# Kernel tuning notes

Measured on AMD Instinct MI355X. Metric: run time of the kernel, lower is better.

The kernel has to match this reference:

```python
import jax, jax.numpy as jnp
import numpy as np

N = 50000          # nodes
E = 800000         # edges (avg degree 16)
D_IN, H1, H2, C = 512, 128, 64, 2
BN_EPS = 1e-5


def gcn_conv(x, w, b, src, dst, deg_inv_sqrt, n):
    """PyG GCNConv (eval): out = D^{-1/2}(A+I)D^{-1/2} (x @ w) + b.
    src/dst already include self-loops; deg_inv_sqrt precomputed on A+I."""
    h = x @ w                                        # [n, out_dim]
    norm = deg_inv_sqrt[src] * deg_inv_sqrt[dst]     # [E+n]
    msgs = h[src] * norm[:, None]                    # gather + scale
    out = jax.ops.segment_sum(msgs, dst, num_segments=n)  # scatter-add
    return out + b


def batch_norm(h, gamma, beta, mean, var):
    return (h - mean) * jax.lax.rsqrt(var + BN_EPS) * gamma + beta


def setup_inputs() -> dict:
    key = jax.random.key(0)
    ks = jax.random.split(key, 18)
    inp = {
        "x": jax.random.normal(ks[0], (N, D_IN), dtype=jnp.float32),
        "edge_index": jax.random.randint(ks[1], (2, E), 0, N, dtype=jnp.int64),
        # layer 1
        "w1": jax.random.normal(ks[2], (D_IN, H1), dtype=jnp.float32) / np.sqrt(D_IN),
        "b1": jnp.zeros((H1,), jnp.float32),
        "g1": jax.random.uniform(ks[3], (H1,), jnp.float32, 0.8, 1.2),
        "beta1": jax.random.normal(ks[4], (H1,), jnp.float32) * 0.1,
        "m1": jax.random.normal(ks[5], (H1,), jnp.float32) * 0.1,
        "v1": jax.random.uniform(ks[6], (H1,), jnp.float32, 0.5, 1.5),
        # layer 2
        "w2": jax.random.normal(ks[7], (H1, H2), dtype=jnp.float32) / np.sqrt(H1),
        "b2": jnp.zeros((H2,), jnp.float32),
        "g2": jax.random.uniform(ks[8], (H2,), jnp.float32, 0.8, 1.2),
        "beta2": jax.random.normal(ks[9], (H2,), jnp.float32) * 0.1,
        "m2": jax.random.normal(ks[10], (H2,), jnp.float32) * 0.1,
        "v2": jax.random.uniform(ks[11], (H2,), jnp.float32, 0.5, 1.5),
        # layer 3
        "w3": jax.random.normal(ks[12], (H2, C), dtype=jnp.float32) / np.sqrt(H2),
        "b3": jnp.zeros((C,), jnp.float32),
    }
    return inp


def reference(x, edge_index, w1, b1, g1, beta1, m1, v1,
              w2, b2, g2, beta2, m2, v2, w3, b3):
    n = x.shape[0]
    loops = jnp.arange(n, dtype=edge_index.dtype)
    src = jnp.concatenate([edge_index[0], loops])   # A + I
    dst = jnp.concatenate([edge_index[1], loops])
    deg = jax.ops.segment_sum(jnp.ones_like(dst, dtype=x.dtype), dst, num_segments=n)
    deg_inv_sqrt = jnp.where(deg > 0, jax.lax.rsqrt(deg), 0.0)

    h = gcn_conv(x, w1, b1, src, dst, deg_inv_sqrt, n)
    h = jax.nn.relu(batch_norm(h, g1, beta1, m1, v1))   # dropout is identity in eval
    h = gcn_conv(h, w2, b2, src, dst, deg_inv_sqrt, n)
    h = jax.nn.relu(batch_norm(h, g2, beta2, m2, v2))
    out = gcn_conv(h, w3, b3, src, dst, deg_inv_sqrt, n)
    return out
```

## Files before the change

### kernel.cpp

```cpp
#include <hip/hip_runtime.h>
#include <hip/hip_fp16.h>


constexpr int NN = 50000;
constexpr int NE = 800000;
constexpr float BN_EPS = 1e-5f;

using f16x8 = __attribute__((ext_vector_type(8))) _Float16;
using f32x4 = __attribute__((ext_vector_type(4))) float;

__global__ void k_prep(const float* __restrict__ w1,
                       const float* __restrict__ b1, const float* __restrict__ g1,
                       const float* __restrict__ beta1, const float* __restrict__ m1,
                       const float* __restrict__ v1,
                       const float* __restrict__ b2, const float* __restrict__ g2,
                       const float* __restrict__ beta2, const float* __restrict__ m2,
                       const float* __restrict__ v2,
                       __half* __restrict__ w1t,
                       float* __restrict__ bns1, float* __restrict__ bnb1,
                       float* __restrict__ bns2, float* __restrict__ bnb2) {
    int i = blockIdx.x * 256 + threadIdx.x;
    if (i < 512 * 128) {
        int k = i >> 7, n = i & 127;
        w1t[n * 512 + k] = __float2half(w1[i]);
    } else if (i < 512 * 128 + 128) {
        int f = i - 512 * 128;
        float s = g1[f] * rsqrtf(v1[f] + BN_EPS);
        bns1[f] = s;
        bnb1[f] = (b1[f] - m1[f]) * s + beta1[f];
    } else if (i < 512 * 128 + 128 + 64) {
        int f = i - (512 * 128 + 128);
        float s = g2[f] * rsqrtf(v2[f] + BN_EPS);
        bns2[f] = s;
        bnb2[f] = (b2[f] - m2[f]) * s + beta2[f];
    }
}


__global__ void k_count(const int* __restrict__ dst, int* __restrict__ cnt, int e) {
    int i = blockIdx.x * 256 + threadIdx.x;
    if (i < e) atomicAdd(&cnt[dst[i]], 1);
}

__global__ __launch_bounds__(1024) void k_scan(const int* __restrict__ cnt,
                                               int* __restrict__ row_start,
                                               float* __restrict__ dis, int n) {
    __shared__ int wsum[16];
    int tid = threadIdx.x;
    int lane = tid & 63, wv = tid >> 6;
    int running = 0;
    if (tid == 0) row_start[0] = 0;
    for (int base = 0; base < n; base += 1024) {
        int c = (base + tid < n) ? cnt[base + tid] : 0;
        if (base + tid < n) dis[base + tid] = rsqrtf((float)(c + 1));
        int v = c;
        #pragma unroll
        for (int off = 1; off < 64; off <<= 1) {
            int t = __shfl_up(v, off);
            if (lane >= off) v += t;
        }
        if (lane == 63) wsum[wv] = v;
        __syncthreads();
        int prefix = 0, total = 0;
        #pragma unroll
        for (int k = 0; k < 16; ++k) {
            int s = wsum[k];
            if (k < wv) prefix += s;
            total += s;
        }
        if (base + tid < n) row_start[base + tid + 1] = running + prefix + v;
        running += total;
        __syncthreads();
    }
}

__global__ void k_fill(const int* __restrict__ src, const int* __restrict__ dst,
                       const int* __restrict__ row_start, int* __restrict__ cnt,
                       int* __restrict__ csr, int e) {
    int i = blockIdx.x * 256 + threadIdx.x;
    if (i < e) {
        int d = dst[i];
        int pos = atomicSub(&cnt[d], 1) - 1;
        csr[row_start[d] + pos] = src[i];
    }
}

__global__ __launch_bounds__(256)
void gemm1_mfma(const float* __restrict__ x, const __half* __restrict__ w1t,
                const float* __restrict__ dis, __half* __restrict__ h1, int M) {
    __shared__ __half As[32][40];
    int tid = threadIdx.x, lane = tid & 63, wv = tid >> 6;
    int bm = blockIdx.x * 32;
    int mh = wv >> 1, nh = wv & 1;

    f32x4 acc[4] = {f32x4{0,0,0,0}, f32x4{0,0,0,0}, f32x4{0,0,0,0}, f32x4{0,0,0,0}};

    const int arow = mh * 16 + (lane & 15);
    const int kgrp = (lane >> 4) * 8;
    const int sr = tid >> 3;
    const int sc = (tid & 7) * 4;
    const bool arow_ok = (bm + sr) < M;
    const float* xrow = x + (size_t)(bm + sr) * 512 + sc;

    for (int k0 = 0; k0 < 512; k0 += 32) {
        float4 v = make_float4(0.f, 0.f, 0.f, 0.f);
        if (arow_ok) v = *reinterpret_cast<const float4*>(xrow + k0);
        __half2* d2 = reinterpret_cast<__half2*>(&As[sr][sc]);
        d2[0] = __floats2half2_rn(v.x, v.y);
        d2[1] = __floats2half2_rn(v.z, v.w);
        __syncthreads();

        f16x8 af = *reinterpret_cast<const f16x8*>(&As[arow][kgrp]);
        #pragma unroll
        for (int t = 0; t < 4; ++t) {
            int col = nh * 64 + t * 16 + (lane & 15);
            f16x8 bf = *reinterpret_cast<const f16x8*>(&w1t[(size_t)col * 512 + k0 + kgrp]);
            acc[t] = __builtin_amdgcn_mfma_f32_16x16x32_f16(af, bf, acc[t], 0, 0, 0);
        }
        __syncthreads();
    }

    #pragma unroll
    for (int j = 0; j < 4; ++j) {
        int row = bm + mh * 16 + (lane >> 4) * 4 + j;
        if (row < M) {
            float dv = dis[row];
            #pragma unroll
            for (int t = 0; t < 4; ++t) {
                int col = nh * 64 + t * 16 + (lane & 15);
                h1[(size_t)row * 128 + col] = __float2half(acc[t][j] * dv);
            }
        }
    }
}


__global__ __launch_bounds__(512)
void agg1_bn_gemm2(const __half* __restrict__ h1, const float* __restrict__ dis,
                   const int* __restrict__ row_start, const int* __restrict__ csr,
                   const float* __restrict__ bns1, const float* __restrict__ bnb1,
                   const float* __restrict__ w2, __half* __restrict__ h2, int n) {
    __shared__ float w2s[128 * 64];
    __shared__ float a1s[8][130];
    int tid = threadIdx.x;
    for (int i = tid; i < 128 * 64 / 4; i += 512)
        reinterpret_cast<float4*>(w2s)[i] = reinterpret_cast<const float4*>(w2)[i];

    int node = (blockIdx.x * 512 + tid) >> 6;
    int lane = tid & 63;
    int wv = tid >> 6;
    float di = 0.f;

    if (node < n) {
        int nd = __builtin_amdgcn_readfirstlane(node);
        di = dis[nd];
        const __half2* hp = reinterpret_cast<const __half2*>(h1);
        float2 hv = __half22float2(hp[(size_t)nd * 64 + lane]);
        float accx = hv.x, accy = hv.y;
        int rs = row_start[nd], re = row_start[nd + 1];
        for (int j = rs; j < re; j += 8) {
            #pragma unroll
            for (int u = 0; u < 8; ++u) {
                int jj = j + u;
                int s = __builtin_amdgcn_readfirstlane(csr[jj < re ? jj : re - 1]);
                float msk = (jj < re) ? 1.f : 0.f;
                float2 f = __half22float2(hp[(size_t)s * 64 + lane]);
                accx += msk * f.x;
                accy += msk * f.y;
            }
        }
        int f0 = lane * 2;
        float y0 = fmaxf(accx * (di * bns1[f0])     + bnb1[f0],     0.f);
        float y1 = fmaxf(accy * (di * bns1[f0 + 1]) + bnb1[f0 + 1], 0.f);
        a1s[wv][f0]     = y0;
        a1s[wv][f0 + 1] = y1;
    }
    __syncthreads();

    if (node < n) {
        float acc = 0.f;
        #pragma unroll
        for (int f = 0; f < 128; f += 4) {
            float a0 = a1s[wv][f + 0], a1v = a1s[wv][f + 1];
            float a2 = a1s[wv][f + 2], a3 = a1s[wv][f + 3];
            acc += a0 * w2s[(f + 0) * 64 + lane];
            acc += a1v * w2s[(f + 1) * 64 + lane];
            acc += a2 * w2s[(f + 2) * 64 + lane];
            acc += a3 * w2s[(f + 3) * 64 + lane];
        }
        h2[(size_t)node * 64 + lane] = __float2half(acc * di);
    }
}

__global__ __launch_bounds__(256)
void agg2_bnrelu_gemm3(const __half* __restrict__ h2, const float* __restrict__ dis,
                       const int* __restrict__ row_start, const int* __restrict__ csr,
                       const float* __restrict__ bns2, const float* __restrict__ bnb2,
                       const float* __restrict__ w3, float* __restrict__ h3, int n) {
    int node = (blockIdx.x * 256 + threadIdx.x) >> 6;
    int lane = threadIdx.x & 63;
    if (node >= n) return;
    int nd = __builtin_amdgcn_readfirstlane(node);
    float di = dis[nd];
    float acc = __half2float(h2[(size_t)nd * 64 + lane]);
    int rs = row_start[nd], re = row_start[nd + 1];
    for (int j = rs; j < re; j += 8) {
        #pragma unroll
        for (int u = 0; u < 8; ++u) {
            int jj = j + u;
            int s = __builtin_amdgcn_readfirstlane(csr[jj < re ? jj : re - 1]);
            float msk = (jj < re) ? 1.f : 0.f;
            acc += msk * __half2float(h2[(size_t)s * 64 + lane]);
        }
    }
    float y = fmaxf(acc * (di * bns2[lane]) + bnb2[lane], 0.f);
    float r0 = y * w3[lane * 2 + 0];
    float r1 = y * w3[lane * 2 + 1];
    #pragma unroll
    for (int off = 32; off > 0; off >>= 1) {
        r0 += __shfl_down(r0, off);
        r1 += __shfl_down(r1, off);
    }
    if (lane == 0) {
        h3[(size_t)nd * 2 + 0] = r0 * di;
        h3[(size_t)nd * 2 + 1] = r1 * di;
    }
}

__global__ void agg3(const float* __restrict__ h3, const float* __restrict__ dis,
                     const int* __restrict__ row_start, const int* __restrict__ csr,
                     const float* __restrict__ b3, float* __restrict__ out, int n) {
    int i = blockIdx.x * 256 + threadIdx.x;
    if (i >= n) return;
    float di = dis[i];
    const float2* hp = reinterpret_cast<const float2*>(h3);
    float2 hv = hp[i];
    float ax = hv.x, ay = hv.y;
    int rs = row_start[i], re = row_start[i + 1];
    for (int j = rs; j < re; j += 8) {
        #pragma unroll
        for (int u = 0; u < 8; ++u) {
            int jj = j + u;
            int s = csr[jj < re ? jj : re - 1];
            float msk = (jj < re) ? 1.f : 0.f;
            float2 v = hp[s];
            ax += msk * v.x;
            ay += msk * v.y;
        }
    }
    out[(size_t)i * 2 + 0] = ax * di + b3[0];
    out[(size_t)i * 2 + 1] = ay * di + b3[1];
}


extern "C" void kernel_launch(void* const* d_in, const int* in_sizes, int n_in,
                              void* d_out, int out_size, void* d_ws, size_t ws_size,
                              hipStream_t stream) {
    const float* x   = (const float*)d_in[0];
    const int*   ei  = (const int*)d_in[1];
    const float* w1  = (const float*)d_in[2];
    const float* b1  = (const float*)d_in[3];
    const float* g1  = (const float*)d_in[4];
    const float* bt1 = (const float*)d_in[5];
    const float* m1  = (const float*)d_in[6];
    const float* v1  = (const float*)d_in[7];
    const float* w2  = (const float*)d_in[8];
    const float* b2  = (const float*)d_in[9];
    const float* g2  = (const float*)d_in[10];
    const float* bt2 = (const float*)d_in[11];
    const float* m2  = (const float*)d_in[12];
    const float* v2  = (const float*)d_in[13];
    const float* w3  = (const float*)d_in[14];
    const float* b3  = (const float*)d_in[15];
    float* out = (float*)d_out;

    const int* srcp = ei;
    const int* dstp = ei + NE;

    char* ws = (char*)d_ws;
    int*    cnt       = (int*)(ws + 0);
    int*    row_start = (int*)(ws + 200064);
    int*    csr       = (int*)(ws + 400128);
    float*  dis       = (float*)(ws + 3600192);
    __half* w1t       = (__half*)(ws + 3800256);
    float*  bns1      = (float*)(ws + 3931392);
    float*  bnb1      = (float*)(ws + 3931904);
    float*  bns2      = (float*)(ws + 3932416);
    float*  bnb2      = (float*)(ws + 3932672);
    __half* h1        = (__half*)(ws + 4000256);
    __half* h2        = (__half*)(ws + 16800512);
    float*  h3        = (float*)(ws + 23200512);

    hipMemsetAsync(cnt, 0, NN * sizeof(int), stream);

    k_prep<<<(512 * 128 + 192 + 255) / 256, 256, 0, stream>>>(
        w1, b1, g1, bt1, m1, v1, b2, g2, bt2, m2, v2, w1t, bns1, bnb1, bns2, bnb2);
    k_count<<<(NE + 255) / 256, 256, 0, stream>>>(dstp, cnt, NE);
    k_scan<<<1, 1024, 0, stream>>>(cnt, row_start, dis, NN);
    k_fill<<<(NE + 255) / 256, 256, 0, stream>>>(srcp, dstp, row_start, cnt, csr, NE);

    gemm1_mfma<<<(NN + 31) / 32, 256, 0, stream>>>(x, w1t, dis, h1, NN);
    agg1_bn_gemm2<<<(NN * 64 + 511) / 512, 512, 0, stream>>>(
        h1, dis, row_start, csr, bns1, bnb1, w2, h2, NN);
    agg2_bnrelu_gemm3<<<(NN * 64 + 255) / 256, 256, 0, stream>>>(
        h2, dis, row_start, csr, bns2, bnb2, w3, h3, NN);
    agg3<<<(NN + 255) / 256, 256, 0, stream>>>(h3, dis, row_start, csr, b3, out, NN);
}
```

Baseline: 451.4 us.

## Split agg1 from gemm2, run gemm2 on MFMA with fragment-packed weights

The fused aggregation-plus-fp32-GEMV kernel is split in two. The aggregation writes fp16 activations to a new buffer, and a new MFMA kernel does the 128x64 GEMM using a weight layout pre-packed into per-lane fragments. The weights for gemm1 are also repacked into fragment order so each lane reads one contiguous 16-byte chunk, and the x tile loads are double-buffered in registers. The aim is to replace the scalar LDS-bound GEMV with tensor-core math and to make the B-operand loads coalesced. The cost is an extra kernel launch, a 12.8 MB intermediate written and read back, and an extra fp16 rounding of the post-BN activations.

```diff
diff --git a/kernel.cpp b/kernel.cpp
--- a/kernel.cpp
+++ b/kernel.cpp
@@ -9,27 +9,39 @@
 using f16x8 = __attribute__((ext_vector_type(8))) _Float16;
 using f32x4 = __attribute__((ext_vector_type(4))) float;
 
-__global__ void k_prep(const float* __restrict__ w1,
+__global__ void k_prep(const float* __restrict__ w1, const float* __restrict__ w2,
                        const float* __restrict__ b1, const float* __restrict__ g1,
                        const float* __restrict__ beta1, const float* __restrict__ m1,
                        const float* __restrict__ v1,
                        const float* __restrict__ b2, const float* __restrict__ g2,
                        const float* __restrict__ beta2, const float* __restrict__ m2,
                        const float* __restrict__ v2,
-                       __half* __restrict__ w1t,
+                       __half* __restrict__ w1f, __half* __restrict__ w2f,
                        float* __restrict__ bns1, float* __restrict__ bnb1,
                        float* __restrict__ bns2, float* __restrict__ bnb2) {
     int i = blockIdx.x * 256 + threadIdx.x;
     if (i < 512 * 128) {
         int k = i >> 7, n = i & 127;
-        w1t[n * 512 + k] = __float2half(w1[i]);
-    } else if (i < 512 * 128 + 128) {
-        int f = i - 512 * 128;
+        int ks = k >> 5, hi = (k & 31) >> 3, j = k & 7;
+        int nh = n >> 6, t = (n >> 4) & 3;
+        int lane = hi * 16 + (n & 15);
+        int slot = ((ks * 2 + nh) * 4 + t) * 64 + lane;
+        w1f[slot * 8 + j] = __float2half(w1[i]);
+    } else if (i < 512 * 128 + 128 * 64) {
+        int i2 = i - 512 * 128;
+        int k = i2 >> 6, n = i2 & 63;
+        int ks = k >> 5, hi = (k & 31) >> 3, j = k & 7;
+        int t = n >> 4;
+        int lane = hi * 16 + (n & 15);
+        int slot = (ks * 4 + t) * 64 + lane;
+        w2f[slot * 8 + j] = __float2half(w2[i2]);
+    } else if (i < 512 * 128 + 128 * 64 + 128) {
+        int f = i - (512 * 128 + 128 * 64);
         float s = g1[f] * rsqrtf(v1[f] + BN_EPS);
         bns1[f] = s;
         bnb1[f] = (b1[f] - m1[f]) * s + beta1[f];
-    } else if (i < 512 * 128 + 128 + 64) {
-        int f = i - (512 * 128 + 128);
+    } else if (i < 512 * 128 + 128 * 64 + 128 + 64) {
+        int f = i - (512 * 128 + 128 * 64 + 128);
         float s = g2[f] * rsqrtf(v2[f] + BN_EPS);
         bns2[f] = s;
         bnb2[f] = (b2[f] - m2[f]) * s + beta2[f];
@@ -86,7 +98,7 @@
 }
 
 __global__ __launch_bounds__(256)
-void gemm1_mfma(const float* __restrict__ x, const __half* __restrict__ w1t,
+void gemm1_mfma(const float* __restrict__ x, const __half* __restrict__ w1f,
                 const float* __restrict__ dis, __half* __restrict__ h1, int M) {
     __shared__ __half As[32][40];
     int tid = threadIdx.x, lane = tid & 63, wv = tid >> 6;
@@ -102,22 +114,28 @@
     const bool arow_ok = (bm + sr) < M;
     const float* xrow = x + (size_t)(bm + sr) * 512 + sc;
 
-    for (int k0 = 0; k0 < 512; k0 += 32) {
-        float4 v = make_float4(0.f, 0.f, 0.f, 0.f);
-        if (arow_ok) v = *reinterpret_cast<const float4*>(xrow + k0);
+    float4 cur = make_float4(0.f, 0.f, 0.f, 0.f);
+    if (arow_ok) cur = *reinterpret_cast<const float4*>(xrow);
+
+    for (int ks = 0; ks < 16; ++ks) {
         __half2* d2 = reinterpret_cast<__half2*>(&As[sr][sc]);
-        d2[0] = __floats2half2_rn(v.x, v.y);
-        d2[1] = __floats2half2_rn(v.z, v.w);
+        d2[0] = __floats2half2_rn(cur.x, cur.y);
+        d2[1] = __floats2half2_rn(cur.z, cur.w);
         __syncthreads();
 
+        float4 nxt = make_float4(0.f, 0.f, 0.f, 0.f);
+        if (ks < 15 && arow_ok)
+            nxt = *reinterpret_cast<const float4*>(xrow + (ks + 1) * 32);
+
         f16x8 af = *reinterpret_cast<const f16x8*>(&As[arow][kgrp]);
         #pragma unroll
         for (int t = 0; t < 4; ++t) {
-            int col = nh * 64 + t * 16 + (lane & 15);
-            f16x8 bf = *reinterpret_cast<const f16x8*>(&w1t[(size_t)col * 512 + k0 + kgrp]);
+            int slot = ((ks * 2 + nh) * 4 + t) * 64 + lane;
+            f16x8 bf = *reinterpret_cast<const f16x8*>(&w1f[slot * 8]);
             acc[t] = __builtin_amdgcn_mfma_f32_16x16x32_f16(af, bf, acc[t], 0, 0, 0);
         }
         __syncthreads();
+        cur = nxt;
     }
 
     #pragma unroll
@@ -134,61 +152,82 @@
     }
 }
 
-
 __global__ __launch_bounds__(512)
-void agg1_bn_gemm2(const __half* __restrict__ h1, const float* __restrict__ dis,
-                   const int* __restrict__ row_start, const int* __restrict__ csr,
-                   const float* __restrict__ bns1, const float* __restrict__ bnb1,
-                   const float* __restrict__ w2, __half* __restrict__ h2, int n) {
-    __shared__ float w2s[128 * 64];
-    __shared__ float a1s[8][130];
-    int tid = threadIdx.x;
-    for (int i = tid; i < 128 * 64 / 4; i += 512)
-        reinterpret_cast<float4*>(w2s)[i] = reinterpret_cast<const float4*>(w2)[i];
-
-    int node = (blockIdx.x * 512 + tid) >> 6;
-    int lane = tid & 63;
-    int wv = tid >> 6;
-    float di = 0.f;
-
-    if (node < n) {
-        int nd = __builtin_amdgcn_readfirstlane(node);
-        di = dis[nd];
-        const __half2* hp = reinterpret_cast<const __half2*>(h1);
-        float2 hv = __half22float2(hp[(size_t)nd * 64 + lane]);
-        float accx = hv.x, accy = hv.y;
-        int rs = row_start[nd], re = row_start[nd + 1];
-        for (int j = rs; j < re; j += 8) {
+void agg1_bn(const __half* __restrict__ h1, const float* __restrict__ dis,
+             const int* __restrict__ row_start, const int* __restrict__ csr,
+             const float* __restrict__ bns1, const float* __restrict__ bnb1,
+             __half* __restrict__ a1, int n) {
+    int node = (blockIdx.x * 512 + threadIdx.x) >> 6;
+    int lane = threadIdx.x & 63;
+    if (node >= n) return;
+    int nd = __builtin_amdgcn_readfirstlane(node);
+    float di = dis[nd];
+    const __half2* hp = reinterpret_cast<const __half2*>(h1);
+    float2 hv = __half22float2(hp[(size_t)nd * 64 + lane]);
+    float accx = hv.x, accy = hv.y;
+    int rs = row_start[nd], re = row_start[nd + 1];
+    for (int j = rs; j < re; j += 8) {
+        #pragma unroll
+        for (int u = 0; u < 8; ++u) {
+            int jj = j + u;
+            int s = __builtin_amdgcn_readfirstlane(csr[jj < re ? jj : re - 1]);
+            float msk = (jj < re) ? 1.f : 0.f;
+            float2 f = __half22float2(hp[(size_t)s * 64 + lane]);
+            accx += msk * f.x;
+            accy += msk * f.y;
+        }
+    }
+    int f0 = lane * 2;
+    float y0 = fmaxf(accx * (di * bns1[f0])     + bnb1[f0],     0.f);
+    float y1 = fmaxf(accy * (di * bns1[f0 + 1]) + bnb1[f0 + 1], 0.f);
+    reinterpret_cast<__half2*>(a1)[(size_t)nd * 64 + lane] = __floats2half2_rn(y0, y1);
+}
+
+__global__ __launch_bounds__(256)
+void gemm2_mfma(const __half* __restrict__ a1, const __half* __restrict__ w2f,
+                const float* __restrict__ dis, __half* __restrict__ h2, int M) {
+    __shared__ __half As[64][136];
+    int tid = threadIdx.x, lane = tid & 63, wv = tid >> 6;
+    int bm = blockIdx.x * 64;
+
+    #pragma unroll
+    for (int p = 0; p < 4; ++p) {
+        int idx = tid + p * 256;
+        int row = idx >> 4;
+        int col = (idx & 15) * 8;
+        f16x8 v = {};
+        if (bm + row < M)
+            v = *reinterpret_cast<const f16x8*>(&a1[(size_t)(bm + row) * 128 + col]);
+        *reinterpret_cast<f16x8*>(&As[row][col]) = v;
+    }
+    __syncthreads();
+
+    f32x4 acc[4] = {f32x4{0,0,0,0}, f32x4{0,0,0,0}, f32x4{0,0,0,0}, f32x4{0,0,0,0}};
+    const int arow = wv * 16 + (lane & 15);
+    const int kgrp = (lane >> 4) * 8;
+
+    #pragma unroll
+    for (int ks = 0; ks < 4; ++ks) {
+        f16x8 af = *reinterpret_cast<const f16x8*>(&As[arow][ks * 32 + kgrp]);
+        #pragma unroll
+        for (int t = 0; t < 4; ++t) {
+            int slot = (ks * 4 + t) * 64 + lane;
+            f16x8 bf = *reinterpret_cast<const f16x8*>(&w2f[slot * 8]);
+            acc[t] = __builtin_amdgcn_mfma_f32_16x16x32_f16(af, bf, acc[t], 0, 0, 0);
+        }
+    }
+
+    #pragma unroll
+    for (int j = 0; j < 4; ++j) {
+        int row = bm + wv * 16 + (lane >> 4) * 4 + j;
+        if (row < M) {
+            float dv = dis[row];
             #pragma unroll
-            for (int u = 0; u < 8; ++u) {
-                int jj = j + u;
-                int s = __builtin_amdgcn_readfirstlane(csr[jj < re ? jj : re - 1]);
-                float msk = (jj < re) ? 1.f : 0.f;
-                float2 f = __half22float2(hp[(size_t)s * 64 + lane]);
-                accx += msk * f.x;
-                accy += msk * f.y;
+            for (int t = 0; t < 4; ++t) {
+                int col = t * 16 + (lane & 15);
+                h2[(size_t)row * 64 + col] = __float2half(acc[t][j] * dv);
             }
         }
-        int f0 = lane * 2;
-        float y0 = fmaxf(accx * (di * bns1[f0])     + bnb1[f0],     0.f);
-        float y1 = fmaxf(accy * (di * bns1[f0 + 1]) + bnb1[f0 + 1], 0.f);
-        a1s[wv][f0]     = y0;
-        a1s[wv][f0 + 1] = y1;
-    }
-    __syncthreads();
-
-    if (node < n) {
-        float acc = 0.f;
-        #pragma unroll
-        for (int f = 0; f < 128; f += 4) {
-            float a0 = a1s[wv][f + 0], a1v = a1s[wv][f + 1];
-            float a2 = a1s[wv][f + 2], a3 = a1s[wv][f + 3];
-            acc += a0 * w2s[(f + 0) * 64 + lane];
-            acc += a1v * w2s[(f + 1) * 64 + lane];
-            acc += a2 * w2s[(f + 2) * 64 + lane];
-            acc += a3 * w2s[(f + 3) * 64 + lane];
-        }
-        h2[(size_t)node * 64 + lane] = __float2half(acc * di);
     }
 }
 
@@ -282,26 +321,30 @@
     int*    row_start = (int*)(ws + 200064);
     int*    csr       = (int*)(ws + 400128);
     float*  dis       = (float*)(ws + 3600192);
-    __half* w1t       = (__half*)(ws + 3800256);
-    float*  bns1      = (float*)(ws + 3931392);
-    float*  bnb1      = (float*)(ws + 3931904);
-    float*  bns2      = (float*)(ws + 3932416);
-    float*  bnb2      = (float*)(ws + 3932672);
+    __half* w1f       = (__half*)(ws + 3800256);
+    __half* w2f       = (__half*)(ws + 3931392);
+    float*  bns1      = (float*)(ws + 3947840);
+    float*  bnb1      = (float*)(ws + 3948352);
+    float*  bns2      = (float*)(ws + 3948864);
+    float*  bnb2      = (float*)(ws + 3949120);
     __half* h1        = (__half*)(ws + 4000256);
-    __half* h2        = (__half*)(ws + 16800512);
-    float*  h3        = (float*)(ws + 23200512);
+    __half* a1        = (__half*)(ws + 16800512);
+    __half* h2        = (__half*)(ws + 29600768);
+    float*  h3        = (float*)(ws + 36000832);
 
     hipMemsetAsync(cnt, 0, NN * sizeof(int), stream);
 
-    k_prep<<<(512 * 128 + 192 + 255) / 256, 256, 0, stream>>>(
-        w1, b1, g1, bt1, m1, v1, b2, g2, bt2, m2, v2, w1t, bns1, bnb1, bns2, bnb2);
+    k_prep<<<(512 * 128 + 128 * 64 + 192 + 255) / 256, 256, 0, stream>>>(
+        w1, w2, b1, g1, bt1, m1, v1, b2, g2, bt2, m2, v2,
+        w1f, w2f, bns1, bnb1, bns2, bnb2);
     k_count<<<(NE + 255) / 256, 256, 0, stream>>>(dstp, cnt, NE);
     k_scan<<<1, 1024, 0, stream>>>(cnt, row_start, dis, NN);
     k_fill<<<(NE + 255) / 256, 256, 0, stream>>>(srcp, dstp, row_start, cnt, csr, NE);
 
-    gemm1_mfma<<<(NN + 31) / 32, 256, 0, stream>>>(x, w1t, dis, h1, NN);
-    agg1_bn_gemm2<<<(NN * 64 + 511) / 512, 512, 0, stream>>>(
-        h1, dis, row_start, csr, bns1, bnb1, w2, h2, NN);
+    gemm1_mfma<<<(NN + 31) / 32, 256, 0, stream>>>(x, w1f, dis, h1, NN);
+    agg1_bn<<<(NN * 64 + 511) / 512, 512, 0, stream>>>(
+        h1, dis, row_start, csr, bns1, bnb1, a1, NN);
+    gemm2_mfma<<<(NN + 63) / 64, 256, 0, stream>>>(a1, w2f, dis, h2, NN);
     agg2_bnrelu_gemm3<<<(NN * 64 + 255) / 256, 256, 0, stream>>>(
         h2, dis, row_start, csr, bns2, bnb2, w3, h3, NN);
     agg3<<<(NN + 255) / 256, 256, 0, stream>>>(h3, dis, row_start, csr, b3, out, NN);
```

Measured after the change: 403.0 us. 10.7% less time.
